# Optimization experiments

Measured on AMD Instinct MI355X. Metric: run time of the kernel, lower is better.

Reference implementation:

```python
import jax, jax.numpy as jnp
import numpy as np
import math

NUM_GRAPHS = 64
NODES_PER_GRAPH = 4096
IN_CHANNELS = 256
AVG_DEGREE = 16
RATIO = 0.5
MULTIPLIER = 1.0


def setup_inputs() -> dict:
    key = jax.random.key(0)
    k1, k2, k3, k4 = jax.random.split(key, 4)
    N = NUM_GRAPHS * NODES_PER_GRAPH
    edges_per_graph = NODES_PER_GRAPH * AVG_DEGREE
    E = NUM_GRAPHS * edges_per_graph
    x = jax.random.normal(k1, (N, IN_CHANNELS), dtype=jnp.float32)
    # edges stay within their own graph (standard torch_geometric batching)
    local = jax.random.randint(k2, (2, NUM_GRAPHS, edges_per_graph), 0,
                               NODES_PER_GRAPH, dtype=jnp.int32)
    offsets = (jnp.arange(NUM_GRAPHS, dtype=jnp.int32) * NODES_PER_GRAPH)[None, :, None]
    edge_index = (local + offsets).reshape(2, E)
    edge_attr = jax.random.normal(k3, (E,), dtype=jnp.float32)
    batch = jnp.repeat(jnp.arange(NUM_GRAPHS, dtype=jnp.int32), NODES_PER_GRAPH)
    weight = jax.random.normal(k4, (1, IN_CHANNELS), dtype=jnp.float32)
    return {"x": x, "edge_index": edge_index, "edge_attr": edge_attr,
            "batch": batch, "weight": weight}


def reference(x, edge_index, edge_attr, batch, weight):
    N = x.shape[0]
    k = math.ceil(RATIO * NODES_PER_GRAPH)
    # score = tanh((x . w) / ||w||)   (min_score is None branch)
    score = jnp.tanh((x * weight).sum(axis=-1) / jnp.linalg.norm(weight))
    # segmented top-k: equal-size graphs -> dense [B, N_per_graph] top_k
    s = score.reshape(NUM_GRAPHS, NODES_PER_GRAPH)
    top_vals, top_idx = jax.lax.top_k(s, k)  # descending per graph, like torch sort
    perm = (top_idx.astype(jnp.int32)
            + (jnp.arange(NUM_GRAPHS, dtype=jnp.int32) * NODES_PER_GRAPH)[:, None]
            ).reshape(-1)  # [B*k] global node ids
    x_out = x[perm] * MULTIPLIER
    batch_out = batch[perm]
    # filter_adj: old->new node id map, keep edges with both endpoints kept
    new_id = jnp.full((N,), -1, dtype=jnp.int32).at[perm].set(
        jnp.arange(perm.shape[0], dtype=jnp.int32))
    nr = new_id[edge_index[0]]
    nc = new_id[edge_index[1]]
    edge_mask = (nr >= 0) & (nc >= 0)
    # fixed-shape (jit-friendly) representation of the filtered edge list:
    # dropped edges get index -1 / attr 0, edge_mask marks kept edges
    edge_index_out = jnp.where(edge_mask[None, :], jnp.stack([nr, nc]), -1)
    edge_attr_out = jnp.where(edge_mask, edge_attr, jnp.zeros((), edge_attr.dtype))
    score_perm = top_vals.reshape(-1)  # == score[perm]
    return (x_out, edge_index_out, edge_attr_out, batch_out, perm, score_perm,
            edge_mask)
```

## Files before the change

kernel.cpp:

```cpp
#include <hip/hip_runtime.h>

#define NG   64
#define NPG  4096
#define C    256
#define NTOT (NG * NPG)
#define K    2048
#define KT   (NG * K)
#define EPG  (NPG * 16)
#define ET   (NG * EPG)

#define OFF_X     0
#define OFF_EI    (KT * C)
#define OFF_ATTR  (OFF_EI + 2 * ET)
#define OFF_BATCH (OFF_ATTR + ET)
#define OFF_PERM  (OFF_BATCH + KT)
#define OFF_SCORE (OFF_PERM + KT)
#define OFF_MASK  (OFF_SCORE + KT)

__device__ __forceinline__ float xla_tanh(float x) {
  float ax = fabsf(x);
  if (ax < 0.0004f) return x;
  const float c = 7.90531110763549805f;
  float t = fminf(fmaxf(x, -c), c);
  float x2 = t * t;
  float p = fmaf(x2, -2.76076847742355e-16f, 2.00018790482477e-13f);
  p = fmaf(x2, p, -8.60467152213735e-11f);
  p = fmaf(x2, p, 5.12229709037114e-08f);
  p = fmaf(x2, p, 1.48572235717979e-05f);
  p = fmaf(x2, p, 6.37261928875436e-04f);
  p = fmaf(x2, p, 4.89352455891786e-03f);
  p = t * p;
  float q = fmaf(x2, 1.19825839466702e-06f, 1.18534705686654e-04f);
  q = fmaf(x2, q, 2.26843463243900e-03f);
  q = fmaf(x2, q, 4.89352518554385e-03f);
  return p / q;
}

__global__ __launch_bounds__(256) void score_kernel(
    const float* __restrict__ x, const float* __restrict__ w,
    float* __restrict__ scores) {
  int node = (int)((blockIdx.x * blockDim.x + threadIdx.x) >> 6);
  int lane = threadIdx.x & 63;
  if (node >= NTOT) return;
  const float4 xv = *reinterpret_cast<const float4*>(x + (size_t)node * C + lane * 4);
  const float4 wv = *reinterpret_cast<const float4*>(w + lane * 4);
  float d = xv.x * wv.x;
  d = fmaf(xv.y, wv.y, d);
  d = fmaf(xv.z, wv.z, d);
  d = fmaf(xv.w, wv.w, d);
  float n = wv.x * wv.x;
  n = fmaf(wv.y, wv.y, n);
  n = fmaf(wv.z, wv.z, n);
  n = fmaf(wv.w, wv.w, n);
  #pragma unroll
  for (int off = 1; off < 64; off <<= 1) {
    d += __shfl_xor(d, off);
    n += __shfl_xor(n, off);
  }
  if (lane == 0) scores[node] = xla_tanh(d / sqrtf(n));
}

__global__ __launch_bounds__(1024) void topk_kernel(
    const float* __restrict__ scores, int* __restrict__ perm_i32,
    int* __restrict__ new_id, float* __restrict__ out) {
  __shared__ unsigned long long keys[NPG];
  const int g = blockIdx.x;
  const int t = threadIdx.x;
  const float* s = scores + g * NPG;

  for (int i = t; i < NPG; i += 1024) {
    unsigned int u = __float_as_uint(s[i]);
    u = (u & 0x80000000u) ? ~u : (u | 0x80000000u);
    u = ~u;
    keys[i] = ((unsigned long long)u << 32) | (unsigned int)i;
  }

  for (int k = 2; k <= NPG; k <<= 1) {
    for (int j = k >> 1; j > 0; j >>= 1) {
      __syncthreads();
      #pragma unroll
      for (int q = 0; q < 2; ++q) {
        int p = t + q * 1024;
        int i = ((p & ~(j - 1)) << 1) | (p & (j - 1));
        int l = i | j;
        unsigned long long a = keys[i], b = keys[l];
        bool up = ((i & k) == 0);
        if ((a > b) == up) { keys[i] = b; keys[l] = a; }
      }
    }
  }
  __syncthreads();

  for (int r = t; r < NPG; r += 1024) {
    int idx = (int)(keys[r] & 0xFFFFFFFFu);
    int node = g * NPG + idx;
    if (r < K) {
      int nid = g * K + r;
      new_id[node] = nid;
      perm_i32[nid] = node;
      out[OFF_BATCH + nid] = (float)g;
      out[OFF_PERM + nid]  = (float)node;
      out[OFF_SCORE + nid] = s[idx];
    } else {
      new_id[node] = -1;
    }
  }
}

__global__ __launch_bounds__(256) void gather_kernel(
    const float* __restrict__ x, const int* __restrict__ perm_i32,
    float* __restrict__ out) {
  int row = (int)((blockIdx.x * blockDim.x + threadIdx.x) >> 6);
  int lane = threadIdx.x & 63;
  if (row >= KT) return;
  int node = perm_i32[row];
  *reinterpret_cast<float4*>(out + OFF_X + (size_t)row * C + lane * 4) =
      *reinterpret_cast<const float4*>(x + (size_t)node * C + lane * 4);
}

__global__ __launch_bounds__(256) void edge_kernel(
    const int* __restrict__ ei, const float* __restrict__ attr,
    const int* __restrict__ new_id, float* __restrict__ out) {
  int t = blockIdx.x * blockDim.x + threadIdx.x;
  if (t >= ET / 4) return;
  int4 r = reinterpret_cast<const int4*>(ei)[t];
  int4 c = reinterpret_cast<const int4*>(ei + ET)[t];
  float4 a = reinterpret_cast<const float4*>(attr)[t];

  int nr[4] = {new_id[r.x], new_id[r.y], new_id[r.z], new_id[r.w]};
  int nc[4] = {new_id[c.x], new_id[c.y], new_id[c.z], new_id[c.w]};
  float4 e0, e1, ao, mo;
  float* e0p = &e0.x; float* e1p = &e1.x; float* aop = &ao.x; float* mop = &mo.x;
  const float* ap = &a.x;
  #pragma unroll
  for (int i = 0; i < 4; ++i) {
    bool keep = (nr[i] >= 0) && (nc[i] >= 0);
    e0p[i] = keep ? (float)nr[i] : -1.0f;
    e1p[i] = keep ? (float)nc[i] : -1.0f;
    aop[i] = keep ? ap[i] : 0.0f;
    mop[i] = keep ? 1.0f : 0.0f;
  }
  reinterpret_cast<float4*>(out + OFF_EI)[t]        = e0;
  reinterpret_cast<float4*>(out + OFF_EI + ET)[t]   = e1;
  reinterpret_cast<float4*>(out + OFF_ATTR)[t]      = ao;
  reinterpret_cast<float4*>(out + OFF_MASK)[t]      = mo;
}

extern "C" void kernel_launch(void* const* d_in, const int* in_sizes, int n_in,
                              void* d_out, int out_size, void* d_ws, size_t ws_size,
                              hipStream_t stream) {
  const float* x    = (const float*)d_in[0];
  const int*   ei   = (const int*)d_in[1];
  const float* attr = (const float*)d_in[2];
  const float* w    = (const float*)d_in[4];
  float* out = (float*)d_out;

  float* scores   = (float*)d_ws;
  int*   perm_i32 = (int*)d_ws + NTOT;
  int*   new_id   = (int*)d_ws + NTOT + KT;

  score_kernel<<<dim3(NTOT * 64 / 256), dim3(256), 0, stream>>>(x, w, scores);
  topk_kernel<<<dim3(NG), dim3(1024), 0, stream>>>(scores, perm_i32, new_id, out);
  gather_kernel<<<dim3(KT * 64 / 256), dim3(256), 0, stream>>>(x, perm_i32, out);
  edge_kernel<<<dim3(ET / 4 / 256), dim3(256), 0, stream>>>(ei, attr, new_id, out);
}
```

Before: 510.9 us.

## Replace bitonic top-k with parallel rank counting and fuse gather with edge filtering

Score kernel now emits sortable 64-bit keys directly. Top-k is computed by having each node count smaller keys within its graph, spreading work over many more blocks instead of a single-block bitonic sort with many barriers. Gather and edge filtering are merged into one launch. This trades O(n^2) comparisons per graph for far better parallelism and no synchronization.

```diff
diff --git a/kernel.cpp b/kernel.cpp
--- a/kernel.cpp
+++ b/kernel.cpp
@@ -38,10 +38,9 @@
 
 __global__ __launch_bounds__(256) void score_kernel(
     const float* __restrict__ x, const float* __restrict__ w,
-    float* __restrict__ scores) {
+    unsigned long long* __restrict__ keys) {
   int node = (int)((blockIdx.x * blockDim.x + threadIdx.x) >> 6);
   int lane = threadIdx.x & 63;
-  if (node >= NTOT) return;
   const float4 xv = *reinterpret_cast<const float4*>(x + (size_t)node * C + lane * 4);
   const float4 wv = *reinterpret_cast<const float4*>(w + lane * 4);
   float d = xv.x * wv.x;
@@ -57,93 +56,85 @@
     d += __shfl_xor(d, off);
     n += __shfl_xor(n, off);
   }
-  if (lane == 0) scores[node] = xla_tanh(d / sqrtf(n));
-}
-
-__global__ __launch_bounds__(1024) void topk_kernel(
-    const float* __restrict__ scores, int* __restrict__ perm_i32,
-    int* __restrict__ new_id, float* __restrict__ out) {
-  __shared__ unsigned long long keys[NPG];
-  const int g = blockIdx.x;
-  const int t = threadIdx.x;
-  const float* s = scores + g * NPG;
-
-  for (int i = t; i < NPG; i += 1024) {
-    unsigned int u = __float_as_uint(s[i]);
+  if (lane == 0) {
+    float s = xla_tanh(d / sqrtf(n));
+    unsigned int u = __float_as_uint(s);
     u = (u & 0x80000000u) ? ~u : (u | 0x80000000u);
     u = ~u;
-    keys[i] = ((unsigned long long)u << 32) | (unsigned int)i;
-  }
-
-  for (int k = 2; k <= NPG; k <<= 1) {
-    for (int j = k >> 1; j > 0; j >>= 1) {
-      __syncthreads();
-      #pragma unroll
-      for (int q = 0; q < 2; ++q) {
-        int p = t + q * 1024;
-        int i = ((p & ~(j - 1)) << 1) | (p & (j - 1));
-        int l = i | j;
-        unsigned long long a = keys[i], b = keys[l];
-        bool up = ((i & k) == 0);
-        if ((a > b) == up) { keys[i] = b; keys[l] = a; }
-      }
-    }
-  }
-  __syncthreads();
-
-  for (int r = t; r < NPG; r += 1024) {
-    int idx = (int)(keys[r] & 0xFFFFFFFFu);
-    int node = g * NPG + idx;
-    if (r < K) {
-      int nid = g * K + r;
-      new_id[node] = nid;
-      perm_i32[nid] = node;
-      out[OFF_BATCH + nid] = (float)g;
-      out[OFF_PERM + nid]  = (float)node;
-      out[OFF_SCORE + nid] = s[idx];
-    } else {
-      new_id[node] = -1;
-    }
+    keys[node] = ((unsigned long long)u << 32) | (unsigned int)(node & (NPG - 1));
   }
 }
 
-__global__ __launch_bounds__(256) void gather_kernel(
-    const float* __restrict__ x, const int* __restrict__ perm_i32,
-    float* __restrict__ out) {
-  int row = (int)((blockIdx.x * blockDim.x + threadIdx.x) >> 6);
-  int lane = threadIdx.x & 63;
-  if (row >= KT) return;
-  int node = perm_i32[row];
-  *reinterpret_cast<float4*>(out + OFF_X + (size_t)row * C + lane * 4) =
-      *reinterpret_cast<const float4*>(x + (size_t)node * C + lane * 4);
+__global__ __launch_bounds__(512) void topk_kernel(
+    const unsigned long long* __restrict__ keys, int* __restrict__ perm_i32,
+    int* __restrict__ new_id, float* __restrict__ out) {
+  const int g = blockIdx.x >> 3;
+  const int i = ((blockIdx.x & 7) << 9) | threadIdx.x;
+  const unsigned long long* kb = keys + g * NPG;
+  const unsigned long long my = kb[i];
+
+  int r0 = 0, r1 = 0, r2 = 0, r3 = 0;
+  #pragma unroll 4
+  for (int j = 0; j < NPG; j += 4) {
+    r0 += (kb[j]     < my);
+    r1 += (kb[j + 1] < my);
+    r2 += (kb[j + 2] < my);
+    r3 += (kb[j + 3] < my);
+  }
+  int rank = (r0 + r1) + (r2 + r3);
+
+  int node = g * NPG + i;
+  if (rank < K) {
+    int nid = g * K + rank;
+    new_id[node] = nid;
+    perm_i32[nid] = node;
+    unsigned int t = ~(unsigned int)(my >> 32);
+    unsigned int su = (t & 0x80000000u) ? (t ^ 0x80000000u) : ~t;
+    out[OFF_BATCH + nid] = (float)g;
+    out[OFF_PERM + nid]  = (float)node;
+    out[OFF_SCORE + nid] = __uint_as_float(su);
+  } else {
+    new_id[node] = -1;
+  }
 }
 
-__global__ __launch_bounds__(256) void edge_kernel(
-    const int* __restrict__ ei, const float* __restrict__ attr,
+#define EBLOCKS (ET / 4 / 256)
+#define GBLOCKS (KT / 4)
+__global__ __launch_bounds__(256) void tail_kernel(
+    const float* __restrict__ x, const int* __restrict__ ei,
+    const float* __restrict__ attr, const int* __restrict__ perm_i32,
     const int* __restrict__ new_id, float* __restrict__ out) {
-  int t = blockIdx.x * blockDim.x + threadIdx.x;
-  if (t >= ET / 4) return;
-  int4 r = reinterpret_cast<const int4*>(ei)[t];
-  int4 c = reinterpret_cast<const int4*>(ei + ET)[t];
-  float4 a = reinterpret_cast<const float4*>(attr)[t];
-
-  int nr[4] = {new_id[r.x], new_id[r.y], new_id[r.z], new_id[r.w]};
-  int nc[4] = {new_id[c.x], new_id[c.y], new_id[c.z], new_id[c.w]};
-  float4 e0, e1, ao, mo;
-  float* e0p = &e0.x; float* e1p = &e1.x; float* aop = &ao.x; float* mop = &mo.x;
-  const float* ap = &a.x;
-  #pragma unroll
-  for (int i = 0; i < 4; ++i) {
-    bool keep = (nr[i] >= 0) && (nc[i] >= 0);
-    e0p[i] = keep ? (float)nr[i] : -1.0f;
-    e1p[i] = keep ? (float)nc[i] : -1.0f;
-    aop[i] = keep ? ap[i] : 0.0f;
-    mop[i] = keep ? 1.0f : 0.0f;
+  int b = blockIdx.x;
+  if (b < EBLOCKS) {
+    int t = b * 256 + threadIdx.x;
+    int4 r = reinterpret_cast<const int4*>(ei)[t];
+    int4 c = reinterpret_cast<const int4*>(ei + ET)[t];
+    float4 a = reinterpret_cast<const float4*>(attr)[t];
+    int nr[4] = {new_id[r.x], new_id[r.y], new_id[r.z], new_id[r.w]};
+    int nc[4] = {new_id[c.x], new_id[c.y], new_id[c.z], new_id[c.w]};
+    float4 e0, e1, ao, mo;
+    float* e0p = &e0.x; float* e1p = &e1.x; float* aop = &ao.x; float* mop = &mo.x;
+    const float* ap = &a.x;
+    #pragma unroll
+    for (int q = 0; q < 4; ++q) {
+      bool keep = (nr[q] >= 0) && (nc[q] >= 0);
+      e0p[q] = keep ? (float)nr[q] : -1.0f;
+      e1p[q] = keep ? (float)nc[q] : -1.0f;
+      aop[q] = keep ? ap[q] : 0.0f;
+      mop[q] = keep ? 1.0f : 0.0f;
+    }
+    reinterpret_cast<float4*>(out + OFF_EI)[t]      = e0;
+    reinterpret_cast<float4*>(out + OFF_EI + ET)[t] = e1;
+    reinterpret_cast<float4*>(out + OFF_ATTR)[t]    = ao;
+    reinterpret_cast<float4*>(out + OFF_MASK)[t]    = mo;
+  } else {
+    int bb = b - EBLOCKS;
+    int row = bb * 4 + (threadIdx.x >> 6);
+    int lane = threadIdx.x & 63;
+    int node = perm_i32[row];
+    *reinterpret_cast<float4*>(out + OFF_X + (size_t)row * C + lane * 4) =
+        *reinterpret_cast<const float4*>(x + (size_t)node * C + lane * 4);
   }
-  reinterpret_cast<float4*>(out + OFF_EI)[t]        = e0;
-  reinterpret_cast<float4*>(out + OFF_EI + ET)[t]   = e1;
-  reinterpret_cast<float4*>(out + OFF_ATTR)[t]      = ao;
-  reinterpret_cast<float4*>(out + OFF_MASK)[t]      = mo;
 }
 
 extern "C" void kernel_launch(void* const* d_in, const int* in_sizes, int n_in,
@@ -155,12 +146,12 @@
   const float* w    = (const float*)d_in[4];
   float* out = (float*)d_out;
 
-  float* scores   = (float*)d_ws;
-  int*   perm_i32 = (int*)d_ws + NTOT;
-  int*   new_id   = (int*)d_ws + NTOT + KT;
+  unsigned long long* keys = (unsigned long long*)d_ws;
+  int* perm_i32 = (int*)d_ws + 2 * NTOT;
+  int* new_id   = (int*)d_ws + 2 * NTOT + KT;
 
-  score_kernel<<<dim3(NTOT * 64 / 256), dim3(256), 0, stream>>>(x, w, scores);
-  topk_kernel<<<dim3(NG), dim3(1024), 0, stream>>>(scores, perm_i32, new_id, out);
-  gather_kernel<<<dim3(KT * 64 / 256), dim3(256), 0, stream>>>(x, perm_i32, out);
-  edge_kernel<<<dim3(ET / 4 / 256), dim3(256), 0, stream>>>(ei, attr, new_id, out);
+  score_kernel<<<dim3(NTOT / 4), dim3(256), 0, stream>>>(x, w, keys);
+  topk_kernel<<<dim3(NG * 8), dim3(512), 0, stream>>>(keys, perm_i32, new_id, out);
+  tail_kernel<<<dim3(EBLOCKS + GBLOCKS), dim3(256), 0, stream>>>(
+      x, ei, attr, perm_i32, new_id, out);
 }
```

After: 565.1 us. 10.6% more time.
